# Kernel tuning notes

Measured on AMD Instinct MI355X. Metric: run time of the kernel, lower is better.

## Reference

```python
import jax, jax.numpy as jnp
import numpy as np


def setup_inputs() -> dict:
    key = jax.random.key(0)
    k1, k2, k3, k4, k5 = jax.random.split(key, 5)
    B, C, H, W = 32, 256, 64, 64
    R = 16  # reduction -> hidden = C // R = 16
    hid = C // R
    return {
        "x": jax.random.normal(k1, (B, C, H, W), dtype=jnp.float32),
        "w1": jax.random.normal(k2, (hid, 1, 1, 1), dtype=jnp.float32) * 0.1,
        "b1": jax.random.normal(k3, (hid,), dtype=jnp.float32) * 0.1,
        "w2": jax.random.normal(k4, (C, hid, 1, 1), dtype=jnp.float32) * 0.1,
        "b2": jax.random.normal(k5, (C,), dtype=jnp.float32) * 0.1,
    }


def reference(x, w1, b1, w2, b2):
    # PositionalAveragePooling: mean over channel dim -> [B, 1, H, W]
    s = jnp.mean(x, axis=1)  # [B, H, W]
    # conv1 (1 -> hid, 1x1): per-position scalar times weight vector + bias
    w1v = w1[:, 0, 0, 0]  # [hid]
    h = jax.nn.relu(s[:, None, :, :] * w1v[None, :, None, None]
                    + b1[None, :, None, None])  # [B, hid, H, W]
    # conv2 (hid -> C, 1x1): pointwise matmul over channel dim
    w2m = w2[:, :, 0, 0]  # [C, hid]
    scale = jax.nn.sigmoid(jnp.einsum("bkhw,ck->bchw", h, w2m)
                           + b2[None, :, None, None])  # [B, C, H, W]
    return x * scale
```

## Files before the change

### kernel.cpp

```cpp
#include <hip/hip_runtime.h>

#define NB 32
#define NC 256
#define NH 64
#define NW 64
#define NK 16
#define HW (NH * NW)

typedef float f32x4 __attribute__((ext_vector_type(4)));

__device__ __forceinline__ float fsig(float z) {
    return __builtin_amdgcn_rcpf(1.0f + __expf(-z));
}

__global__ __launch_bounds__(1024, 8) void pse_kernel(
    const float* __restrict__ x,
    const float* __restrict__ w1,
    const float* __restrict__ b1,
    const float* __restrict__ w2,
    const float* __restrict__ b2,
    float* __restrict__ out)
{
    __shared__ float w2t[NK][NC + 4];
    __shared__ f32x4 part[64][17];
    __shared__ f32x4 sA[16][17];
    __shared__ f32x4 hv4[NK][16];
    __shared__ float b2s[NC];

    const int t  = threadIdx.x;
    const int cg = t >> 4;
    const int q  = t & 15;

    const int bh = blockIdx.x;
    const int b  = bh >> 6;
    const int h  = bh & 63;

    const size_t base = (size_t)b * NC * HW + (size_t)h * NW;
    const float* __restrict__ xp = x + base;
    float* __restrict__ op       = out + base;
    const float* __restrict__ xr = xp + (size_t)(cg << 2) * HW + (q << 2);

    f32x4 xv[4];
    #pragma unroll
    for (int i = 0; i < 4; ++i)
        xv[i] = __builtin_nontemporal_load(
            reinterpret_cast<const f32x4*>(xr + (size_t)i * HW));

    {
        const f32x4 v = reinterpret_cast<const f32x4*>(w2)[t];
        const int c  = t >> 2;
        const int k0 = (t & 3) << 2;
        w2t[k0 + 0][c] = v.x;
        w2t[k0 + 1][c] = v.y;
        w2t[k0 + 2][c] = v.z;
        w2t[k0 + 3][c] = v.w;
        if (t < NC) b2s[t] = b2[t];
    }

    part[cg][q] = xv[0] + xv[1] + xv[2] + xv[3];
    __syncthreads();

    if (t < 256) {
        const int a = t >> 4;
        sA[a][q] = part[4 * a + 0][q] + part[4 * a + 1][q]
                 + part[4 * a + 2][q] + part[4 * a + 3][q];
    }
    __syncthreads();

    if (t < 256) {
        const int k = t >> 4;
        f32x4 s = (f32x4)(0.f);
        #pragma unroll
        for (int i = 0; i < 16; ++i) s += sA[i][q];
        s *= (1.0f / (float)NC);
        const float w1k = w1[k];
        const float b1k = b1[k];
        f32x4 hv;
        hv.x = fmaxf(fmaf(s.x, w1k, b1k), 0.f);
        hv.y = fmaxf(fmaf(s.y, w1k, b1k), 0.f);
        hv.z = fmaxf(fmaf(s.z, w1k, b1k), 0.f);
        hv.w = fmaxf(fmaf(s.w, w1k, b1k), 0.f);
        hv4[k][q] = hv;
    }
    __syncthreads();

    f32x4 acc[4];
    #pragma unroll
    for (int i = 0; i < 4; ++i) acc[i] = (f32x4)(b2s[(cg << 2) + i]);

    #pragma unroll
    for (int k = 0; k < NK; ++k) {
        const f32x4 hk = hv4[k][q];
        const f32x4 wv = *reinterpret_cast<const f32x4*>(&w2t[k][cg << 2]);
        acc[0] += hk * wv.x;
        acc[1] += hk * wv.y;
        acc[2] += hk * wv.z;
        acc[3] += hk * wv.w;
    }

    #pragma unroll
    for (int i = 0; i < 4; ++i) {
        const f32x4 xvv = xv[i];
        f32x4 r;
        r.x = xvv.x * fsig(acc[i].x);
        r.y = xvv.y * fsig(acc[i].y);
        r.z = xvv.z * fsig(acc[i].z);
        r.w = xvv.w * fsig(acc[i].w);
        __builtin_nontemporal_store(r,
            reinterpret_cast<f32x4*>(op + (size_t)((cg << 2) + i) * HW + (q << 2)));
    }
}

extern "C" void kernel_launch(void* const* d_in, const int* in_sizes, int n_in,
                              void* d_out, int out_size, void* d_ws, size_t ws_size,
                              hipStream_t stream) {
    const float* x  = (const float*)d_in[0];
    const float* w1 = (const float*)d_in[1];
    const float* b1 = (const float*)d_in[2];
    const float* w2 = (const float*)d_in[3];
    const float* b2 = (const float*)d_in[4];
    float* out = (float*)d_out;

    dim3 grid(NB * NH);
    dim3 block(1024);
    hipLaunchKernelGGL(pse_kernel, grid, block, 0, stream, x, w1, b1, w2, b2, out);
}
```

Baseline: 228.8 us.

## Split fused kernel into separate channel-mean and apply kernels using workspace

```diff
diff --git a/kernel.cpp b/kernel.cpp
--- a/kernel.cpp
+++ b/kernel.cpp
@@ -13,12 +13,78 @@
     return __builtin_amdgcn_rcpf(1.0f + __expf(-z));
 }
 
-__global__ __launch_bounds__(1024, 8) void pse_kernel(
+__global__ __launch_bounds__(256, 8) void pse_mean(
+    const float* __restrict__ x, float* __restrict__ s)
+{
+    __shared__ f32x4 part[16][17];
+    const int t  = threadIdx.x;
+    const int cg = t >> 4;
+    const int q  = t & 15;
+
+    const int bh = blockIdx.x;
+    const int b  = bh >> 6;
+    const int h  = bh & 63;
+
+    const float* __restrict__ xr =
+        x + (size_t)b * NC * HW + (size_t)(cg << 4) * HW + (size_t)h * NW + (q << 2);
+
+    f32x4 p = (f32x4)(0.f);
+    #pragma unroll
+    for (int i = 0; i < 16; ++i)
+        p += *reinterpret_cast<const f32x4*>(xr + (size_t)i * HW);
+    part[cg][q] = p;
+    __syncthreads();
+
+    if (t < 16) {
+        f32x4 acc = (f32x4)(0.f);
+        #pragma unroll
+        for (int i = 0; i < 16; ++i) acc += part[i][t];
+        acc *= (1.0f / (float)NC);
+        reinterpret_cast<f32x4*>(s)[bh * 16 + t] = acc;
+    }
+}
+
+__global__ __launch_bounds__(256, 8) void pse_apply(
+    const float* __restrict__ x, const float* __restrict__ s,
+    const float* __restrict__ w1, const float* __restrict__ b1,
+    const float* __restrict__ w2, const float* __restrict__ b2,
+    float* __restrict__ out)
+{
+    const int t  = threadIdx.x;
+    const int w  = t & 63;
+    const int cg = __builtin_amdgcn_readfirstlane(t >> 6);
+
+    const int bh = blockIdx.x;
+    const int b  = bh >> 6;
+    const int h  = bh & 63;
+
+    const float sv = s[bh * NW + w];
+    float hv[NK];
+    #pragma unroll
+    for (int k = 0; k < NK; ++k)
+        hv[k] = fmaxf(fmaf(sv, w1[k], b1[k]), 0.f);
+
+    const size_t base = (size_t)b * NC * HW + (size_t)(cg << 6) * HW
+                      + (size_t)h * NW + w;
+    const float* __restrict__ xp = x + base;
+    float* __restrict__ op       = out + base;
+
+    #pragma unroll 8
+    for (int c = 0; c < 64; ++c) {
+        const float xvv = xp[(size_t)c * HW];
+        const int ch = (cg << 6) + c;
+        const float* __restrict__ wr = w2 + ch * NK;
+        float acc = b2[ch];
+        #pragma unroll
+        for (int k = 0; k < NK; ++k) acc = fmaf(hv[k], wr[k], acc);
+        __builtin_nontemporal_store(xvv * fsig(acc), op + (size_t)c * HW);
+    }
+}
+
+__global__ __launch_bounds__(1024, 8) void pse_fused(
     const float* __restrict__ x,
-    const float* __restrict__ w1,
-    const float* __restrict__ b1,
-    const float* __restrict__ w2,
-    const float* __restrict__ b2,
+    const float* __restrict__ w1, const float* __restrict__ b1,
+    const float* __restrict__ w2, const float* __restrict__ b2,
     float* __restrict__ out)
 {
     __shared__ float w2t[NK][NC + 4];
@@ -30,7 +96,6 @@
     const int t  = threadIdx.x;
     const int cg = t >> 4;
     const int q  = t & 15;
-
     const int bh = blockIdx.x;
     const int b  = bh >> 6;
     const int h  = bh & 63;
@@ -50,36 +115,30 @@
         const f32x4 v = reinterpret_cast<const f32x4*>(w2)[t];
         const int c  = t >> 2;
         const int k0 = (t & 3) << 2;
-        w2t[k0 + 0][c] = v.x;
-        w2t[k0 + 1][c] = v.y;
-        w2t[k0 + 2][c] = v.z;
-        w2t[k0 + 3][c] = v.w;
+        w2t[k0 + 0][c] = v.x; w2t[k0 + 1][c] = v.y;
+        w2t[k0 + 2][c] = v.z; w2t[k0 + 3][c] = v.w;
         if (t < NC) b2s[t] = b2[t];
     }
 
     part[cg][q] = xv[0] + xv[1] + xv[2] + xv[3];
     __syncthreads();
-
     if (t < 256) {
         const int a = t >> 4;
-        sA[a][q] = part[4 * a + 0][q] + part[4 * a + 1][q]
-                 + part[4 * a + 2][q] + part[4 * a + 3][q];
+        sA[a][q] = part[4*a][q] + part[4*a+1][q] + part[4*a+2][q] + part[4*a+3][q];
     }
     __syncthreads();
-
     if (t < 256) {
         const int k = t >> 4;
-        f32x4 s = (f32x4)(0.f);
+        f32x4 ssum = (f32x4)(0.f);
         #pragma unroll
-        for (int i = 0; i < 16; ++i) s += sA[i][q];
-        s *= (1.0f / (float)NC);
-        const float w1k = w1[k];
-        const float b1k = b1[k];
+        for (int i = 0; i < 16; ++i) ssum += sA[i][q];
+        ssum *= (1.0f / (float)NC);
+        const float w1k = w1[k], b1k = b1[k];
         f32x4 hv;
-        hv.x = fmaxf(fmaf(s.x, w1k, b1k), 0.f);
-        hv.y = fmaxf(fmaf(s.y, w1k, b1k), 0.f);
-        hv.z = fmaxf(fmaf(s.z, w1k, b1k), 0.f);
-        hv.w = fmaxf(fmaf(s.w, w1k, b1k), 0.f);
+        hv.x = fmaxf(fmaf(ssum.x, w1k, b1k), 0.f);
+        hv.y = fmaxf(fmaf(ssum.y, w1k, b1k), 0.f);
+        hv.z = fmaxf(fmaf(ssum.z, w1k, b1k), 0.f);
+        hv.w = fmaxf(fmaf(ssum.w, w1k, b1k), 0.f);
         hv4[k][q] = hv;
     }
     __syncthreads();
@@ -87,17 +146,13 @@
     f32x4 acc[4];
     #pragma unroll
     for (int i = 0; i < 4; ++i) acc[i] = (f32x4)(b2s[(cg << 2) + i]);
-
     #pragma unroll
     for (int k = 0; k < NK; ++k) {
         const f32x4 hk = hv4[k][q];
         const f32x4 wv = *reinterpret_cast<const f32x4*>(&w2t[k][cg << 2]);
-        acc[0] += hk * wv.x;
-        acc[1] += hk * wv.y;
-        acc[2] += hk * wv.z;
-        acc[3] += hk * wv.w;
+        acc[0] += hk * wv.x; acc[1] += hk * wv.y;
+        acc[2] += hk * wv.z; acc[3] += hk * wv.w;
     }
-
     #pragma unroll
     for (int i = 0; i < 4; ++i) {
         const f32x4 xvv = xv[i];
@@ -121,7 +176,14 @@
     const float* b2 = (const float*)d_in[4];
     float* out = (float*)d_out;
 
-    dim3 grid(NB * NH);
-    dim3 block(1024);
-    hipLaunchKernelGGL(pse_kernel, grid, block, 0, stream, x, w1, b1, w2, b2, out);
+    const size_t s_bytes = (size_t)NB * NH * NW * sizeof(float);
+    if (ws_size >= s_bytes) {
+        float* s = (float*)d_ws;
+        hipLaunchKernelGGL(pse_mean,  dim3(NB * NH), dim3(256), 0, stream, x, s);
+        hipLaunchKernelGGL(pse_apply, dim3(NB * NH), dim3(256), 0, stream,
+                           x, s, w1, b1, w2, b2, out);
+    } else {
+        hipLaunchKernelGGL(pse_fused, dim3(NB * NH), dim3(1024), 0, stream,
+                           x, w1, b1, w2, b2, out);
+    }
 }
```

Measured after the change: 259.0 us. 1.13x slower.

## Make blocks persistent over several rows with double-buffered prefetch

Applied to the files above, without the earlier changes.

```diff
diff --git a/kernel.cpp b/kernel.cpp
--- a/kernel.cpp
+++ b/kernel.cpp
@@ -6,6 +6,8 @@
 #define NW 64
 #define NK 16
 #define HW (NH * NW)
+#define NIT 8
+#define NBLK (NB * NH / NIT)
 
 typedef float f32x4 __attribute__((ext_vector_type(4)));
 
@@ -13,7 +15,7 @@
     return __builtin_amdgcn_rcpf(1.0f + __expf(-z));
 }
 
-__global__ __launch_bounds__(1024, 8) void pse_kernel(
+__global__ __launch_bounds__(1024, 4) void pse_kernel(
     const float* __restrict__ x,
     const float* __restrict__ w1,
     const float* __restrict__ b1,
@@ -22,93 +24,106 @@
     float* __restrict__ out)
 {
     __shared__ float w2t[NK][NC + 4];
-    __shared__ f32x4 part[64][17];
-    __shared__ f32x4 sA[16][17];
+    __shared__ f32x4 part[16][17];
     __shared__ f32x4 hv4[NK][16];
     __shared__ float b2s[NC];
 
-    const int t  = threadIdx.x;
-    const int cg = t >> 4;
-    const int q  = t & 15;
-
-    const int bh = blockIdx.x;
-    const int b  = bh >> 6;
-    const int h  = bh & 63;
-
-    const size_t base = (size_t)b * NC * HW + (size_t)h * NW;
-    const float* __restrict__ xp = x + base;
-    float* __restrict__ op       = out + base;
-    const float* __restrict__ xr = xp + (size_t)(cg << 2) * HW + (q << 2);
-
-    f32x4 xv[4];
-    #pragma unroll
-    for (int i = 0; i < 4; ++i)
-        xv[i] = __builtin_nontemporal_load(
-            reinterpret_cast<const f32x4*>(xr + (size_t)i * HW));
+    const int t   = threadIdx.x;
+    const int cg  = t >> 4;
+    const int q   = t & 15;
+    const int wid = t >> 6;
+    const int blk = blockIdx.x;
 
     {
         const f32x4 v = reinterpret_cast<const f32x4*>(w2)[t];
         const int c  = t >> 2;
         const int k0 = (t & 3) << 2;
-        w2t[k0 + 0][c] = v.x;
-        w2t[k0 + 1][c] = v.y;
-        w2t[k0 + 2][c] = v.z;
-        w2t[k0 + 3][c] = v.w;
+        w2t[k0 + 0][c] = v.x; w2t[k0 + 1][c] = v.y;
+        w2t[k0 + 2][c] = v.z; w2t[k0 + 3][c] = v.w;
         if (t < NC) b2s[t] = b2[t];
     }
+    float w1k = 0.f, b1k = 0.f;
+    if (t < 256) { const int k = t >> 4; w1k = w1[k]; b1k = b1[k]; }
 
-    part[cg][q] = xv[0] + xv[1] + xv[2] + xv[3];
-    __syncthreads();
+    const size_t lane_off = (size_t)(cg << 2) * HW + (q << 2);
 
-    if (t < 256) {
-        const int a = t >> 4;
-        sA[a][q] = part[4 * a + 0][q] + part[4 * a + 1][q]
-                 + part[4 * a + 2][q] + part[4 * a + 3][q];
-    }
-    __syncthreads();
+    f32x4 xv[2][4];
 
-    if (t < 256) {
-        const int k = t >> 4;
-        f32x4 s = (f32x4)(0.f);
-        #pragma unroll
-        for (int i = 0; i < 16; ++i) s += sA[i][q];
-        s *= (1.0f / (float)NC);
-        const float w1k = w1[k];
-        const float b1k = b1[k];
-        f32x4 hv;
-        hv.x = fmaxf(fmaf(s.x, w1k, b1k), 0.f);
-        hv.y = fmaxf(fmaf(s.y, w1k, b1k), 0.f);
-        hv.z = fmaxf(fmaf(s.z, w1k, b1k), 0.f);
-        hv.w = fmaxf(fmaf(s.w, w1k, b1k), 0.f);
-        hv4[k][q] = hv;
-    }
-    __syncthreads();
+#define ROWPTR(IT, BASE) \
+    ((BASE) + (size_t)((((IT) << 8) + blk) >> 6) * NC * HW \
+            + (size_t)((((IT) << 8) + blk) & 63) * NW + lane_off)
 
-    f32x4 acc[4];
-    #pragma unroll
-    for (int i = 0; i < 4; ++i) acc[i] = (f32x4)(b2s[(cg << 2) + i]);
+#define LOADROW(BUF, IT) { \
+    const float* _p = ROWPTR(IT, x); \
+    _Pragma("unroll") \
+    for (int _i = 0; _i < 4; ++_i) \
+        BUF[_i] = __builtin_nontemporal_load( \
+            reinterpret_cast<const f32x4*>(_p + (size_t)_i * HW)); }
+
+    LOADROW(xv[0], 0)
 
     #pragma unroll
-    for (int k = 0; k < NK; ++k) {
-        const f32x4 hk = hv4[k][q];
-        const f32x4 wv = *reinterpret_cast<const f32x4*>(&w2t[k][cg << 2]);
-        acc[0] += hk * wv.x;
-        acc[1] += hk * wv.y;
-        acc[2] += hk * wv.z;
-        acc[3] += hk * wv.w;
+    for (int it = 0; it < NIT; ++it) {
+        const int cur = it & 1, nxt = cur ^ 1;
+
+        if (it + 1 < NIT) LOADROW(xv[nxt], it + 1)
+
+        {
+            f32x4 p = xv[cur][0] + xv[cur][1] + xv[cur][2] + xv[cur][3];
+            p.x += __shfl_xor(p.x, 16, 64); p.y += __shfl_xor(p.y, 16, 64);
+            p.z += __shfl_xor(p.z, 16, 64); p.w += __shfl_xor(p.w, 16, 64);
+            p.x += __shfl_xor(p.x, 32, 64); p.y += __shfl_xor(p.y, 32, 64);
+            p.z += __shfl_xor(p.z, 32, 64); p.w += __shfl_xor(p.w, 32, 64);
+            if ((t & 63) < 16) part[wid][q] = p;
+        }
+        __syncthreads();
+
+        if (t < 256) {
+            f32x4 s = (f32x4)(0.f);
+            #pragma unroll
+            for (int i = 0; i < 16; ++i) s += part[i][q];
+            s *= (1.0f / (float)NC);
+            f32x4 hv;
+            hv.x = fmaxf(fmaf(s.x, w1k, b1k), 0.f);
+            hv.y = fmaxf(fmaf(s.y, w1k, b1k), 0.f);
+            hv.z = fmaxf(fmaf(s.z, w1k, b1k), 0.f);
+            hv.w = fmaxf(fmaf(s.w, w1k, b1k), 0.f);
+            hv4[t >> 4][q] = hv;
+        }
+        __syncthreads();
+
+        {
+            f32x4 acc0 = (f32x4)(b2s[(cg << 2) + 0]);
+            f32x4 acc1 = (f32x4)(b2s[(cg << 2) + 1]);
+            f32x4 acc2 = (f32x4)(b2s[(cg << 2) + 2]);
+            f32x4 acc3 = (f32x4)(b2s[(cg << 2) + 3]);
+            #pragma unroll
+            for (int k = 0; k < NK; ++k) {
+                const f32x4 hk = hv4[k][q];
+                const f32x4 wvv = *reinterpret_cast<const f32x4*>(&w2t[k][cg << 2]);
+                acc0 += hk * wvv.x; acc1 += hk * wvv.y;
+                acc2 += hk * wvv.z; acc3 += hk * wvv.w;
+            }
+            float* _o = const_cast<float*>(ROWPTR(it, out));
+            const f32x4 xc0 = xv[cur][0], xc1 = xv[cur][1];
+            const f32x4 xc2 = xv[cur][2], xc3 = xv[cur][3];
+            f32x4 r;
+            r.x = xc0.x * fsig(acc0.x); r.y = xc0.y * fsig(acc0.y);
+            r.z = xc0.z * fsig(acc0.z); r.w = xc0.w * fsig(acc0.w);
+            __builtin_nontemporal_store(r, reinterpret_cast<f32x4*>(_o + 0 * (size_t)HW));
+            r.x = xc1.x * fsig(acc1.x); r.y = xc1.y * fsig(acc1.y);
+            r.z = xc1.z * fsig(acc1.z); r.w = xc1.w * fsig(acc1.w);
+            __builtin_nontemporal_store(r, reinterpret_cast<f32x4*>(_o + 1 * (size_t)HW));
+            r.x = xc2.x * fsig(acc2.x); r.y = xc2.y * fsig(acc2.y);
+            r.z = xc2.z * fsig(acc2.z); r.w = xc2.w * fsig(acc2.w);
+            __builtin_nontemporal_store(r, reinterpret_cast<f32x4*>(_o + 2 * (size_t)HW));
+            r.x = xc3.x * fsig(acc3.x); r.y = xc3.y * fsig(acc3.y);
+            r.z = xc3.z * fsig(acc3.z); r.w = xc3.w * fsig(acc3.w);
+            __builtin_nontemporal_store(r, reinterpret_cast<f32x4*>(_o + 3 * (size_t)HW));
+        }
     }
-
-    #pragma unroll
-    for (int i = 0; i < 4; ++i) {
-        const f32x4 xvv = xv[i];
-        f32x4 r;
-        r.x = xvv.x * fsig(acc[i].x);
-        r.y = xvv.y * fsig(acc[i].y);
-        r.z = xvv.z * fsig(acc[i].z);
-        r.w = xvv.w * fsig(acc[i].w);
-        __builtin_nontemporal_store(r,
-            reinterpret_cast<f32x4*>(op + (size_t)((cg << 2) + i) * HW + (q << 2)));
-    }
+#undef LOADROW
+#undef ROWPTR
 }
 
 extern "C" void kernel_launch(void* const* d_in, const int* in_sizes, int n_in,
@@ -121,7 +136,6 @@
     const float* b2 = (const float*)d_in[4];
     float* out = (float*)d_out;
 
-    dim3 grid(NB * NH);
-    dim3 block(1024);
-    hipLaunchKernelGGL(pse_kernel, grid, block, 0, stream, x, w1, b1, w2, b2, out);
+    hipLaunchKernelGGL(pse_kernel, dim3(NBLK), dim3(1024), 0, stream,
+                       x, w1, b1, w2, b2, out);
 }
```

New measurement: 234.6 us. 1.03x slower.
